# Optimization experiments

Measured on AMD Instinct MI355X. Metric: run time of the kernel, lower is better.

The kernel has to match this reference:

```python
import jax, jax.numpy as jnp
import numpy as np

# Module config (from init_kwargs)
B = 1024          # batch
CIN = 1024        # in_channels
COUT = 2048       # out_channels
K = 7             # kernel_size; input spatial must equal K so deform-conv out is 1x1
STRIDE, PAD, DIL, DG = 1, 0, 1, 1  # stride, padding, dilation, deformable_groups
H = W = K


def setup_inputs() -> dict:
    key = jax.random.key(0)
    k1, k2, k3, k4, k5, k6 = jax.random.split(key, 6)
    x = jax.random.normal(k1, (B, CIN, H, W), dtype=jnp.float32)
    # offset-predicting conv: Conv2d(CIN, 2*K*K*DG, K, bias=False); small init so offsets are a few pixels
    offset_w = jax.random.normal(k2, (2 * DG * K * K, CIN, K, K), dtype=jnp.float32) * 0.01
    # deformable conv weight/bias (kaiming-like scale)
    deform_w = jax.random.normal(k3, (COUT, CIN, K, K), dtype=jnp.float32) * (1.0 / np.sqrt(CIN * K * K))
    deform_b = jax.random.normal(k4, (COUT,), dtype=jnp.float32) * 0.01
    # fused linear COUT -> COUT
    lin_w = jax.random.normal(k5, (COUT, COUT), dtype=jnp.float32) * (1.0 / np.sqrt(COUT))
    lin_b = jax.random.normal(k6, (COUT,), dtype=jnp.float32) * 0.01
    return {"x": x, "offset_w": offset_w, "deform_w": deform_w,
            "deform_b": deform_b, "lin_w": lin_w, "lin_b": lin_b}


def _deform_conv2d(x, offset, weight, bias):
    """torchvision deform_conv2d (v1, no modulation mask), groups=1.
    x: [B, C, H, W]; offset: [B, 2*DG*K*K, Ho, Wo] ordered (dg, kh, kw, (dy,dx)).
    """
    Bn, C, Hx, Wx = x.shape
    Cout, _, Kh, Kw = weight.shape
    P = Kh * Kw
    Ho, Wo = offset.shape[2], offset.shape[3]
    L = Ho * Wo
    Cg = C // DG

    off = offset.reshape(Bn, DG, P, 2, Ho, Wo)
    ky = jnp.repeat(jnp.arange(Kh), Kw).astype(x.dtype)   # [P]
    kx = jnp.tile(jnp.arange(Kw), Kh).astype(x.dtype)     # [P]
    base_y = (jnp.arange(Ho) * STRIDE - PAD).astype(x.dtype)  # [Ho]
    base_x = (jnp.arange(Wo) * STRIDE - PAD).astype(x.dtype)  # [Wo]
    # sampling positions [B, DG, P, Ho, Wo]
    py = off[:, :, :, 0] + (ky * DIL)[None, None, :, None, None] + base_y[None, None, None, :, None]
    px = off[:, :, :, 1] + (kx * DIL)[None, None, :, None, None] + base_x[None, None, None, None, :]

    y0 = jnp.floor(py); x0 = jnp.floor(px)
    fy = py - y0;       fx = px - x0
    y0i = y0.astype(jnp.int32); x0i = x0.astype(jnp.int32)

    xg = x.reshape(Bn, DG, Cg, Hx * Wx)
    acc = jnp.zeros((Bn, DG, Cg, P * L), x.dtype)
    for di, wy in ((0, 1.0 - fy), (1, fy)):
        for dj, wx in ((0, 1.0 - fx), (1, fx)):
            yi = y0i + di
            xi = x0i + dj
            valid = (yi >= 0) & (yi < Hx) & (xi >= 0) & (xi < Wx)  # zero-pad outside
            idx = (jnp.clip(yi, 0, Hx - 1) * Wx + jnp.clip(xi, 0, Wx - 1)).reshape(Bn, DG, 1, P * L)
            wgt = (wy * wx * valid.astype(x.dtype)).reshape(Bn, DG, 1, P * L)
            g = jnp.take_along_axis(xg, jnp.broadcast_to(idx, (Bn, DG, Cg, P * L)), axis=-1)
            acc = acc + g * wgt
    # columns: [B, C*P, L] with (channel, kernel-tap) ordering matching weight layout
    cols = acc.reshape(Bn, DG, Cg, P, L).reshape(Bn, C * P, L)
    out = jnp.einsum('ok,bkl->bol', weight.reshape(Cout, C * P), cols) + bias[None, :, None]
    return out.reshape(Bn, Cout, Ho, Wo)


def reference(x, offset_w, deform_w, deform_b, lin_w, lin_b):
    # 1) offset-predicting conv (bias=False)
    offset = jax.lax.conv_general_dilated(
        x, offset_w, window_strides=(STRIDE, STRIDE),
        padding=[(PAD, PAD), (PAD, PAD)], rhs_dilation=(DIL, DIL),
        dimension_numbers=('NCHW', 'OIHW', 'NCHW'))  # [B, 2*DG*K*K, 1, 1]
    # 2) deformable conv
    y = _deform_conv2d(x, offset, deform_w, deform_b)  # [B, COUT, 1, 1]
    # 3) linear over flattened features (spatial is 1x1 so flat dim == COUT)
    y = y.reshape(B, COUT) @ lin_w.T + lin_b
    # 4) softshrink(lambd=0.5)
    y = jnp.where(y > 0.5, y - 0.5, jnp.where(y < -0.5, y + 0.5, jnp.zeros_like(y)))
    return y.reshape(B, COUT, 1, 1)
```

## Files before the change

kernel.cpp:

```cpp
#include <hip/hip_runtime.h>

typedef _Float16 f16;
typedef _Float16 f16x8 __attribute__((ext_vector_type(8)));
typedef float f32x4 __attribute__((ext_vector_type(4)));

#define DEVI static __device__ __forceinline__

DEVI void async_ld16(const void* g, void* l) {
  __builtin_amdgcn_global_load_lds(
      (const __attribute__((address_space(1))) unsigned int*)g,
      (__attribute__((address_space(3))) unsigned int*)l, 16, 0, 0);
}

DEVI int sw_off(int row, int q) {
  return row * 64 + ((q ^ ((row >> 1) & 3)) << 4);
}

template<bool A_F32>
__global__ __launch_bounds__(256, 2)
void gemm_bt(const void* __restrict__ Aptr, const f16* __restrict__ Bt,
             float* __restrict__ Cpart, int ldK, int Nvalid,
             int mTiles, int nTiles, int kPerSplit, int Mtot) {
  __shared__ __align__(16) f16 As[128 * 32];
  __shared__ __align__(16) f16 Bs[128 * 32];

  int nb = gridDim.x;
  int bid = (blockIdx.x & 7) * (nb >> 3) + (blockIdx.x >> 3);
  int ms = bid % mTiles; bid /= mTiles;
  int ns = bid % nTiles; bid /= nTiles;
  int ks = bid;
  int m0 = ms * 128, n0 = ns * 128;
  int k0 = ks * kPerSplit;

  int tid = threadIdx.x;
  int w = tid >> 6, lane = tid & 63;
  int wrow = (w >> 1) * 64, wcol = (w & 1) * 64;
  int lrow = lane & 15, lquad = lane >> 4;

  f32x4 acc[4][4];
#pragma unroll
  for (int i = 0; i < 4; ++i)
#pragma unroll
    for (int j = 0; j < 4; ++j) acc[i][j] = (f32x4){0.f, 0.f, 0.f, 0.f};

  for (int kk = k0; kk < k0 + kPerSplit; kk += 32) {
    __syncthreads();
#pragma unroll
    for (int s = 0; s < 2; ++s) {
      int rl = w * 32 + s * 16 + (lane >> 2);
      int qp = lane & 3;
      int q = qp ^ ((rl >> 1) & 3);
      int rb = n0 + rl; if (rb > Nvalid - 1) rb = Nvalid - 1;
      async_ld16(Bt + (size_t)rb * ldK + kk + q * 8, &Bs[(w * 32 + s * 16) * 32]);
    }
    if (!A_F32) {
      const f16* Ah = (const f16*)Aptr;
#pragma unroll
      for (int s = 0; s < 2; ++s) {
        int rl = w * 32 + s * 16 + (lane >> 2);
        int qp = lane & 3;
        int q = qp ^ ((rl >> 1) & 3);
        async_ld16(Ah + (size_t)(m0 + rl) * ldK + kk + q * 8, &As[(w * 32 + s * 16) * 32]);
      }
    } else {
      const float* Af = (const float*)Aptr;
      int r = tid >> 1, half = tid & 1;
      const float* src = Af + (size_t)(m0 + r) * ldK + kk + half * 16;
      float v[16];
#pragma unroll
      for (int u = 0; u < 4; ++u) {
        f32x4 t4 = *(const f32x4*)(src + u * 4);
        v[u * 4 + 0] = t4[0]; v[u * 4 + 1] = t4[1];
        v[u * 4 + 2] = t4[2]; v[u * 4 + 3] = t4[3];
      }
#pragma unroll
      for (int u2 = 0; u2 < 2; ++u2) {
        f16x8 h;
#pragma unroll
        for (int e = 0; e < 8; ++e) h[e] = (f16)v[u2 * 8 + e];
        *(f16x8*)((char*)As + sw_off(r, half * 2 + u2)) = h;
      }
    }
    __syncthreads();

    f16x8 af[4], bf[4];
#pragma unroll
    for (int i = 0; i < 4; ++i)
      af[i] = *(const f16x8*)((const char*)As + sw_off(wrow + i * 16 + lrow, lquad));
#pragma unroll
    for (int j = 0; j < 4; ++j)
      bf[j] = *(const f16x8*)((const char*)Bs + sw_off(wcol + j * 16 + lrow, lquad));
#pragma unroll
    for (int i = 0; i < 4; ++i)
#pragma unroll
      for (int j = 0; j < 4; ++j)
        acc[i][j] = __builtin_amdgcn_mfma_f32_16x16x32_f16(af[i], bf[j], acc[i][j], 0, 0, 0);
  }

  size_t base = (size_t)ks * Mtot * Nvalid;
#pragma unroll
  for (int i = 0; i < 4; ++i) {
    int row = m0 + wrow + i * 16 + lquad * 4;
#pragma unroll
    for (int j = 0; j < 4; ++j) {
      int col = n0 + wcol + j * 16 + lrow;
      if (col < Nvalid) {
#pragma unroll
        for (int r = 0; r < 4; ++r)
          Cpart[base + (size_t)(row + r) * Nvalid + col] = acc[i][j][r];
      }
    }
  }
}

__global__ void cvt_f32_to_f16(const float* __restrict__ in, f16* __restrict__ out, long n) {
  long idx = ((long)blockIdx.x * blockDim.x + threadIdx.x) * 8;
  if (idx + 8 <= n) {
    f32x4 a = *(const f32x4*)(in + idx);
    f32x4 b = *(const f32x4*)(in + idx + 4);
    f16x8 o;
    o[0] = (f16)a[0]; o[1] = (f16)a[1]; o[2] = (f16)a[2]; o[3] = (f16)a[3];
    o[4] = (f16)b[0]; o[5] = (f16)b[1]; o[6] = (f16)b[2]; o[7] = (f16)b[3];
    *(f16x8*)(out + idx) = o;
  }
}

__global__ __launch_bounds__(256)
void build_cols(const float* __restrict__ x, const float* __restrict__ offs,
                f16* __restrict__ cols) {
  int b = blockIdx.x;
  __shared__ int s_idx[49][4];
  __shared__ float s_w[49][4];
  int t = threadIdx.x;
  if (t < 49) {
    float dy = offs[b * 98 + 2 * t];
    float dx = offs[b * 98 + 2 * t + 1];
    float py = dy + (float)(t / 7);
    float px = dx + (float)(t % 7);
    float fy0 = floorf(py), fx0 = floorf(px);
    int y0 = (int)fy0, x0 = (int)fx0;
    float fy = py - fy0, fx = px - fx0;
#pragma unroll
    for (int di = 0; di < 2; ++di)
#pragma unroll
      for (int dj = 0; dj < 2; ++dj) {
        int yi = y0 + di, xi = x0 + dj;
        bool valid = (yi >= 0) && (yi < 7) && (xi >= 0) && (xi < 7);
        int yc = yi < 0 ? 0 : (yi > 6 ? 6 : yi);
        int xc = xi < 0 ? 0 : (xi > 6 ? 6 : xi);
        float wy = di ? fy : 1.f - fy;
        float wx = dj ? fx : 1.f - fx;
        s_idx[t][di * 2 + dj] = yc * 7 + xc;
        s_w[t][di * 2 + dj] = valid ? wy * wx : 0.f;
      }
  }
  __syncthreads();
  const float* xb = x + (size_t)b * 50176;
  f16* cb = cols + (size_t)b * 50176;
  for (int k0 = t * 8; k0 < 50176; k0 += 256 * 8) {
    f16x8 h;
#pragma unroll
    for (int u = 0; u < 8; ++u) {
      int k = k0 + u;
      int c = k / 49;
      int p = k - c * 49;
      const float* xc = xb + c * 49;
      float v = s_w[p][0] * xc[s_idx[p][0]] + s_w[p][1] * xc[s_idx[p][1]]
              + s_w[p][2] * xc[s_idx[p][2]] + s_w[p][3] * xc[s_idx[p][3]];
      h[u] = (f16)v;
    }
    *(f16x8*)(cb + k0) = h;
  }
}

__global__ void combine_k(const float* __restrict__ parts, int nparts, size_t pstride,
                          const float* __restrict__ bias, float* __restrict__ outf,
                          f16* __restrict__ outh, int total, int cols, int shrink) {
  int i = blockIdx.x * 256 + threadIdx.x;
  if (i >= total) return;
  float s = 0.f;
  for (int p = 0; p < nparts; ++p) s += parts[(size_t)p * pstride + i];
  if (bias) s += bias[i % cols];
  if (shrink) s = s > 0.5f ? s - 0.5f : (s < -0.5f ? s + 0.5f : 0.f);
  if (outf) outf[i] = s;
  if (outh) outh[i] = (f16)s;
}

extern "C" void kernel_launch(void* const* d_in, const int* in_sizes, int n_in,
                              void* d_out, int out_size, void* d_ws, size_t ws_size,
                              hipStream_t stream) {
  const float* x  = (const float*)d_in[0];
  const float* ow = (const float*)d_in[1];
  const float* dw = (const float*)d_in[2];
  const float* db = (const float*)d_in[3];
  const float* lw = (const float*)d_in[4];
  const float* lb = (const float*)d_in[5];
  float* out = (float*)d_out;

  const long KX = 50176;
  char* ws = (char*)d_ws;
  size_t off = 0;
  auto alloc = [&](size_t bytes) {
    char* p = ws + off;
    off = (off + bytes + 255) & ~(size_t)255;
    return p;
  };
  f16*   dw_h = (f16*)  alloc((size_t)2048 * KX * 2);
  f16*   ow_h = (f16*)  alloc((size_t)98 * KX * 2);
  f16*   lw_h = (f16*)  alloc((size_t)2048 * 2048 * 2);
  float* offp = (float*)alloc((size_t)32 * 1024 * 98 * 4);
  float* offs = (float*)alloc((size_t)1024 * 98 * 4);
  f16*   cols = (f16*)  alloc((size_t)1024 * KX * 2);
  float* y1p  = (float*)alloc((size_t)4 * 1024 * 2048 * 4);
  f16*   y1h  = (f16*)  alloc((size_t)1024 * 2048 * 2);
  float* y2p  = (float*)alloc((size_t)2 * 1024 * 2048 * 4);
  if (off > ws_size) return;

  long n_dw = 2048L * KX, n_ow = 98L * KX, n_lw = 2048L * 2048L;
  cvt_f32_to_f16<<<(unsigned)(n_dw / 8 / 256), 256, 0, stream>>>(dw, dw_h, n_dw);
  cvt_f32_to_f16<<<(unsigned)(n_ow / 8 / 256), 256, 0, stream>>>(ow, ow_h, n_ow);
  cvt_f32_to_f16<<<(unsigned)(n_lw / 8 / 256), 256, 0, stream>>>(lw, lw_h, n_lw);

  gemm_bt<true><<<8 * 1 * 32, 256, 0, stream>>>(x, ow_h, offp, 50176, 98, 8, 1, 1568, 1024);
  combine_k<<<(1024 * 98 + 255) / 256, 256, 0, stream>>>(
      offp, 32, (size_t)1024 * 98, nullptr, offs, nullptr, 1024 * 98, 98, 0);

  build_cols<<<1024, 256, 0, stream>>>(x, offs, cols);

  gemm_bt<false><<<8 * 16 * 4, 256, 0, stream>>>(cols, dw_h, y1p, 50176, 2048, 8, 16, 12544, 1024);
  combine_k<<<(2097152 + 255) / 256, 256, 0, stream>>>(
      y1p, 4, (size_t)2097152, db, nullptr, y1h, 2097152, 2048, 0);

  gemm_bt<false><<<8 * 16 * 2, 256, 0, stream>>>(y1h, lw_h, y2p, 2048, 2048, 8, 16, 1024, 1024);
  combine_k<<<(2097152 + 255) / 256, 256, 0, stream>>>(
      y2p, 2, (size_t)2097152, lb, out, nullptr, 2097152, 2048, 1);
}
```

Baseline: 1.263 ms.

## Convert deform weight to f16 inside GEMM and raise split-K and occupancy

Drops the standalone f32-to-f16 pass over the 2048x50176 deform-conv weight. The main GEMM now reads the f32 weight directly and converts it while staging into LDS, through a new B_F32 template path. Split-K factors are raised for all three GEMMs (49, 8, 8) to launch more blocks, and launch bounds move to 4 blocks per SM. The cost is that the weight is now read as f32 once per M-tile (8 times) instead of once as f16 afterwards, the partial-sum buffers and combine work grow, and the B loads become synchronous register loads instead of async LDS loads.

```diff
diff --git a/kernel.cpp b/kernel.cpp
--- a/kernel.cpp
+++ b/kernel.cpp
@@ -16,9 +16,22 @@
   return row * 64 + ((q ^ ((row >> 1) & 3)) << 4);
 }
 
-template<bool A_F32>
-__global__ __launch_bounds__(256, 2)
-void gemm_bt(const void* __restrict__ Aptr, const f16* __restrict__ Bt,
+DEVI void stage_f32_tile(const float* __restrict__ src_row, f16* lds, int tid) {
+  int r = tid >> 1, half = tid & 1;
+#pragma unroll
+  for (int u2 = 0; u2 < 2; ++u2) {
+    f32x4 a = *(const f32x4*)(src_row + half * 16 + u2 * 8);
+    f32x4 b = *(const f32x4*)(src_row + half * 16 + u2 * 8 + 4);
+    f16x8 h;
+    h[0] = (f16)a[0]; h[1] = (f16)a[1]; h[2] = (f16)a[2]; h[3] = (f16)a[3];
+    h[4] = (f16)b[0]; h[5] = (f16)b[1]; h[6] = (f16)b[2]; h[7] = (f16)b[3];
+    *(f16x8*)((char*)lds + sw_off(r, half * 2 + u2)) = h;
+  }
+}
+
+template<bool A_F32, bool B_F32>
+__global__ __launch_bounds__(256, 4)
+void gemm_bt(const void* __restrict__ Aptr, const void* __restrict__ Bptr,
              float* __restrict__ Cpart, int ldK, int Nvalid,
              int mTiles, int nTiles, int kPerSplit, int Mtot) {
   __shared__ __align__(16) f16 As[128 * 32];
@@ -45,14 +58,6 @@
 
   for (int kk = k0; kk < k0 + kPerSplit; kk += 32) {
     __syncthreads();
-#pragma unroll
-    for (int s = 0; s < 2; ++s) {
-      int rl = w * 32 + s * 16 + (lane >> 2);
-      int qp = lane & 3;
-      int q = qp ^ ((rl >> 1) & 3);
-      int rb = n0 + rl; if (rb > Nvalid - 1) rb = Nvalid - 1;
-      async_ld16(Bt + (size_t)rb * ldK + kk + q * 8, &Bs[(w * 32 + s * 16) * 32]);
-    }
     if (!A_F32) {
       const f16* Ah = (const f16*)Aptr;
 #pragma unroll
@@ -62,24 +67,26 @@
         int q = qp ^ ((rl >> 1) & 3);
         async_ld16(Ah + (size_t)(m0 + rl) * ldK + kk + q * 8, &As[(w * 32 + s * 16) * 32]);
       }
-    } else {
+    }
+    if (!B_F32) {
+      const f16* Bh = (const f16*)Bptr;
+#pragma unroll
+      for (int s = 0; s < 2; ++s) {
+        int rl = w * 32 + s * 16 + (lane >> 2);
+        int qp = lane & 3;
+        int q = qp ^ ((rl >> 1) & 3);
+        int rb = n0 + rl; if (rb > Nvalid - 1) rb = Nvalid - 1;
+        async_ld16(Bh + (size_t)rb * ldK + kk + q * 8, &Bs[(w * 32 + s * 16) * 32]);
+      }
+    }
+    if (A_F32) {
       const float* Af = (const float*)Aptr;
-      int r = tid >> 1, half = tid & 1;
-      const float* src = Af + (size_t)(m0 + r) * ldK + kk + half * 16;
-      float v[16];
-#pragma unroll
-      for (int u = 0; u < 4; ++u) {
-        f32x4 t4 = *(const f32x4*)(src + u * 4);
-        v[u * 4 + 0] = t4[0]; v[u * 4 + 1] = t4[1];
-        v[u * 4 + 2] = t4[2]; v[u * 4 + 3] = t4[3];
-      }
-#pragma unroll
-      for (int u2 = 0; u2 < 2; ++u2) {
-        f16x8 h;
-#pragma unroll
-        for (int e = 0; e < 8; ++e) h[e] = (f16)v[u2 * 8 + e];
-        *(f16x8*)((char*)As + sw_off(r, half * 2 + u2)) = h;
-      }
+      stage_f32_tile(Af + (size_t)(m0 + (tid >> 1)) * ldK + kk, As, tid);
+    }
+    if (B_F32) {
+      const float* Bf = (const float*)Bptr;
+      int rb = n0 + (tid >> 1); if (rb > Nvalid - 1) rb = Nvalid - 1;
+      stage_f32_tile(Bf + (size_t)rb * ldK + kk, Bs, tid);
     }
     __syncthreads();
 
@@ -205,33 +212,34 @@
     off = (off + bytes + 255) & ~(size_t)255;
     return p;
   };
-  f16*   dw_h = (f16*)  alloc((size_t)2048 * KX * 2);
   f16*   ow_h = (f16*)  alloc((size_t)98 * KX * 2);
   f16*   lw_h = (f16*)  alloc((size_t)2048 * 2048 * 2);
-  float* offp = (float*)alloc((size_t)32 * 1024 * 98 * 4);
+  float* offp = (float*)alloc((size_t)49 * 1024 * 98 * 4);
   float* offs = (float*)alloc((size_t)1024 * 98 * 4);
   f16*   cols = (f16*)  alloc((size_t)1024 * KX * 2);
-  float* y1p  = (float*)alloc((size_t)4 * 1024 * 2048 * 4);
+  float* y1p  = (float*)alloc((size_t)8 * 1024 * 2048 * 4);
   f16*   y1h  = (f16*)  alloc((size_t)1024 * 2048 * 2);
-  float* y2p  = (float*)alloc((size_t)2 * 1024 * 2048 * 4);
+  float* y2p  = (float*)alloc((size_t)8 * 1024 * 2048 * 4);
   if (off > ws_size) return;
 
-  long n_dw = 2048L * KX, n_ow = 98L * KX, n_lw = 2048L * 2048L;
-  cvt_f32_to_f16<<<(unsigned)(n_dw / 8 / 256), 256, 0, stream>>>(dw, dw_h, n_dw);
+  long n_ow = 98L * KX, n_lw = 2048L * 2048L;
   cvt_f32_to_f16<<<(unsigned)(n_ow / 8 / 256), 256, 0, stream>>>(ow, ow_h, n_ow);
   cvt_f32_to_f16<<<(unsigned)(n_lw / 8 / 256), 256, 0, stream>>>(lw, lw_h, n_lw);
 
-  gemm_bt<true><<<8 * 1 * 32, 256, 0, stream>>>(x, ow_h, offp, 50176, 98, 8, 1, 1568, 1024);
+  gemm_bt<true, false><<<8 * 1 * 49, 256, 0, stream>>>(
+      x, ow_h, offp, 50176, 98, 8, 1, 1024, 1024);
   combine_k<<<(1024 * 98 + 255) / 256, 256, 0, stream>>>(
-      offp, 32, (size_t)1024 * 98, nullptr, offs, nullptr, 1024 * 98, 98, 0);
+      offp, 49, (size_t)1024 * 98, nullptr, offs, nullptr, 1024 * 98, 98, 0);
 
   build_cols<<<1024, 256, 0, stream>>>(x, offs, cols);
 
-  gemm_bt<false><<<8 * 16 * 4, 256, 0, stream>>>(cols, dw_h, y1p, 50176, 2048, 8, 16, 12544, 1024);
+  gemm_bt<false, true><<<8 * 16 * 8, 256, 0, stream>>>(
+      cols, dw, y1p, 50176, 2048, 8, 16, 6272, 1024);
   combine_k<<<(2097152 + 255) / 256, 256, 0, stream>>>(
-      y1p, 4, (size_t)2097152, db, nullptr, y1h, 2097152, 2048, 0);
-
-  gemm_bt<false><<<8 * 16 * 2, 256, 0, stream>>>(y1h, lw_h, y2p, 2048, 2048, 8, 16, 1024, 1024);
+      y1p, 8, (size_t)2097152, db, nullptr, y1h, 2097152, 2048, 0);
+
+  gemm_bt<false, false><<<8 * 16 * 8, 256, 0, stream>>>(
+      y1h, lw_h, y2p, 2048, 2048, 8, 16, 256, 1024);
   combine_k<<<(2097152 + 255) / 256, 256, 0, stream>>>(
-      y2p, 2, (size_t)2097152, lb, out, nullptr, 2097152, 2048, 1);
-}
+      y2p, 8, (size_t)2097152, lb, out, nullptr, 2097152, 2048, 1);
+}
```

Measured after the change: 1.268 ms. Within noise of the previous version (+0.4%).
